# Performance work log

Hardware: AMD Instinct MI355X
Metric: run time of the kernel (lower is better)

## Reference

```python
import jax, jax.numpy as jnp
import numpy as np

B, S, D, DA, H = 4, 2048, 1024, 1024, 16
DH = DA // H  # 64, per-head dim (tensor_split on last dim == contiguous head chunks)


def setup_inputs() -> dict:
    key = jax.random.key(0)
    ks = jax.random.split(key, 8)
    init = 0.02
    return {
        "q": jax.random.normal(ks[0], (B, S, D), jnp.float32),
        "k": jax.random.normal(ks[1], (B, S, D), jnp.float32),
        "v": jax.random.normal(ks[2], (B, S, D), jnp.float32),
        "mask": jnp.ones((B, 1, S), jnp.int32),
        "w_q": jax.random.normal(ks[3], (DA, D), jnp.float32) * init,
        "b_q": jnp.zeros((DA,), jnp.float32),
        "w_k": jax.random.normal(ks[4], (DA, D), jnp.float32) * init,
        "b_k": jnp.zeros((DA,), jnp.float32),
        "w_v": jax.random.normal(ks[5], (DA, D), jnp.float32) * init,
        "b_v": jnp.zeros((DA,), jnp.float32),
        "w_o": jax.random.normal(ks[6], (D, DA), jnp.float32) * init,
        "b_o": jnp.zeros((D,), jnp.float32),
    }


def reference(q, k, v, mask, w_q, b_q, w_k, b_k, w_v, b_v, w_o, b_o):
    # projections (nn.Linear: x @ W.T + b)
    xq = q @ w_q.T + b_q            # [B,S,DA]
    xk = k @ w_k.T + b_k
    xv = v @ w_v.T + b_v
    # tensor_split into h contiguous chunks == reshape to [B,S,H,DH]
    xq = xq.reshape(B, S, H, DH)
    xk = xk.reshape(B, S, H, DH)
    xv = xv.reshape(B, S, H, DH)
    scores = jnp.einsum('bqhd,bkhd->bhqk', xq, xk) / jnp.sqrt(jnp.asarray(DH, xq.dtype))
    # mask [B,1,S] broadcasts over heads and query rows -> [B,1,1,S]
    scores = jnp.where(mask[:, None] == 0, -jnp.inf, scores)
    probs = jax.nn.softmax(scores, axis=-1)  # dropout p=0.0 -> identity
    out = jnp.einsum('bhqk,bkhd->bqhd', probs, xv).reshape(B, S, DA)
    return out @ w_o.T + b_o        # [B,S,D]
```

## Files before the change

### kernel.cpp

```cpp
#include <hip/hip_runtime.h>
#include <hip/hip_bf16.h>
#include <cstdint>
#include <cstddef>

typedef __bf16 bf16;
typedef __attribute__((ext_vector_type(8))) __bf16 bf16x8;
typedef __attribute__((ext_vector_type(4))) __bf16 bf16x4;
typedef __attribute__((ext_vector_type(4))) float f32x4;
typedef __attribute__((ext_vector_type(4))) int i32x4;

#define MFMA_BF16(a, b, c) __builtin_amdgcn_mfma_f32_16x16x32_bf16((a), (b), (c), 0, 0, 0)

constexpr int CB = 4;
constexpr int CS = 2048;
constexpr int CD = 1024;
constexpr int CDA = 1024;
constexpr int CH = 16;
constexpr int CM = CB * CS;
constexpr int NT = CS / 64;

__global__ __launch_bounds__(256) void cvt_w4(
    const float* __restrict__ s0, const float* __restrict__ s1,
    const float* __restrict__ s2, const float* __restrict__ s3,
    bf16* __restrict__ dst)
{
    int bid = blockIdx.x;
    int m = bid >> 9;
    size_t li = ((size_t)(bid & 511) * 256 + threadIdx.x) * 8;
    const float* s = (m == 0) ? s0 : (m == 1) ? s1 : (m == 2) ? s2 : s3;
    f32x4 a = *(const f32x4*)(s + li);
    f32x4 c = *(const f32x4*)(s + li + 4);
    bf16x8 o;
#pragma unroll
    for (int j = 0; j < 4; ++j) { o[j] = (bf16)a[j]; o[4 + j] = (bf16)c[j]; }
    *(bf16x8*)(dst + (size_t)m * (CD * CDA) + li) = o;
}

struct P3 {
    const float *A0, *A1, *A2;
    const float *b0, *b1, *b2;
    bf16 *C0, *C1, *C2;
};

__global__ __launch_bounds__(512, 2) void gemm_proj(P3 p, const bf16* __restrict__ Wb)
{
    __shared__ __align__(16) char smem[98304];

    const int t = threadIdx.x;
    const int lane = t & 63;
    const int wid = t >> 6;
    const int wr = wid >> 2, wc = wid & 3;
    const int l15 = lane & 15, lg = lane >> 4;
    const int m0 = blockIdx.x * 128;
    const int n0 = blockIdx.y * 256;
    const int z = blockIdx.z;

    const float* A    = (z == 0) ? p.A0 : (z == 1) ? p.A1 : p.A2;
    const float* bias = (z == 0) ? p.b0 : (z == 1) ? p.b1 : p.b2;
    const bf16*  W    = Wb + (size_t)z * (CD * CDA);

    const int arow = t >> 2, aq = t & 3;
    const float* asrc = A + (size_t)(m0 + arow) * CD + aq * 16;
    const int aoff0 = arow * 128 + (((2 * aq) ^ (arow & 7)) << 4);
    const int aoff1 = arow * 128 + (((2 * aq + 1) ^ (arow & 7)) << 4);
    const int brow_ = wid * 8 + (lane >> 3);
    const int bcol = ((lane & 7) ^ ((lane >> 3) & 7)) << 3;

    f32x4 av0, av1, av2, av3;

    auto ALOAD = [&](int k0) {
        av0 = *(const f32x4*)(asrc + k0);
        av1 = *(const f32x4*)(asrc + k0 + 4);
        av2 = *(const f32x4*)(asrc + k0 + 8);
        av3 = *(const f32x4*)(asrc + k0 + 12);
    };
    auto AWRITE = [&](int bufi) {
        char* Ab = smem + bufi * 16384;
        bf16x8 o0, o1;
#pragma unroll
        for (int jj = 0; jj < 4; ++jj) {
            o0[jj] = (bf16)av0[jj]; o0[4 + jj] = (bf16)av1[jj];
            o1[jj] = (bf16)av2[jj]; o1[4 + jj] = (bf16)av3[jj];
        }
        *(bf16x8*)(Ab + aoff0) = o0;
        *(bf16x8*)(Ab + aoff1) = o1;
    };
    auto BSTAGE = [&](int bufi, int k0) {
        char* Bb = smem + 32768 + bufi * 32768;
#pragma unroll
        for (int i = 0; i < 4; ++i) {
            const bf16* src = W + (size_t)(n0 + i * 64 + brow_) * CD + k0 + bcol;
            __builtin_amdgcn_global_load_lds(
                (const __attribute__((address_space(1))) void*)src,
                (__attribute__((address_space(3))) void*)(Bb + i * 8192 + wid * 1024),
                16, 0, 0);
        }
    };

    f32x4 acc[4][4] = {};

    ALOAD(0); BSTAGE(0, 0); AWRITE(0);
    __syncthreads();

    for (int ks = 0; ks < CD / 64; ++ks) {
        const int cur = ks & 1;
        if (ks + 1 < CD / 64) { BSTAGE(cur ^ 1, (ks + 1) * 64); ALOAD((ks + 1) * 64); }
        char* Ab = smem + cur * 16384;
        char* Bb = smem + 32768 + cur * 32768;
#pragma unroll
        for (int kk = 0; kk < 64; kk += 32) {
            bf16x8 af[4], bfv[4];
#pragma unroll
            for (int mi = 0; mi < 4; ++mi) {
                int row = wr * 64 + mi * 16 + l15;
                af[mi] = *(const bf16x8*)(Ab + row * 128 +
                                          ((((kk >> 3) + lg) ^ (row & 7)) << 4));
            }
#pragma unroll
            for (int ni = 0; ni < 4; ++ni) {
                int row = wc * 64 + ni * 16 + l15;
                bfv[ni] = *(const bf16x8*)(Bb + 128 * row +
                                           ((((kk >> 3) + lg) ^ (row & 7)) << 4));
            }
            __builtin_amdgcn_s_setprio(1);
#pragma unroll
            for (int mi = 0; mi < 4; ++mi)
#pragma unroll
                for (int ni = 0; ni < 4; ++ni)
                    acc[mi][ni] = MFMA_BF16(af[mi], bfv[ni], acc[mi][ni]);
            __builtin_amdgcn_s_setprio(0);
        }
        if (ks + 1 < CD / 64) AWRITE(cur ^ 1);
        __syncthreads();
    }

    if (z == 2) {
        bf16* C = p.C2;
        const int mblock = m0 + wr * 64;
#pragma unroll
        for (int ni = 0; ni < 4; ++ni) {
            int n = n0 + wc * 64 + ni * 16 + l15;
            float bv = bias[n];
#pragma unroll
            for (int mi = 0; mi < 4; ++mi) {
                int s = mi * 16 + lg * 4;
                int cps = (s & 32) | ((s & 12) << 1) | ((s & 16) >> 2);
                bf16x4 o;
#pragma unroll
                for (int r = 0; r < 4; ++r) o[r] = (bf16)(acc[mi][ni][r] + bv);
                *(bf16x4*)(C + (size_t)n * CM + mblock + cps) = o;
            }
        }
    } else {
        bf16* C = (z == 0) ? p.C0 : p.C1;
#pragma unroll
        for (int ni = 0; ni < 4; ++ni) {
            int col = n0 + wc * 64 + ni * 16 + l15;
            float bv = bias[col];
#pragma unroll
            for (int mi = 0; mi < 4; ++mi)
#pragma unroll
                for (int r = 0; r < 4; ++r) {
                    int row = m0 + wr * 64 + mi * 16 + lg * 4 + r;
                    C[(size_t)row * CDA + col] = (bf16)(acc[mi][ni][r] + bv);
                }
        }
    }
}

__global__ __launch_bounds__(512, 2) void gemm_out(
    const bf16* __restrict__ A, const bf16* __restrict__ W,
    const float* __restrict__ bias, float* __restrict__ C)
{
    __shared__ __align__(16) char smem[98304];

    const int t = threadIdx.x;
    const int lane = t & 63;
    const int wid = t >> 6;
    const int wr = wid >> 2, wc = wid & 3;
    const int l15 = lane & 15, lg = lane >> 4;
    const int m0 = blockIdx.x * 128;
    const int n0 = blockIdx.y * 256;

    const int grow_ = wid * 8 + (lane >> 3);
    const int gcol = ((lane & 7) ^ ((lane >> 3) & 7)) << 3;

    auto STAGE = [&](int bufi, int k0) {
        char* Ab = smem + bufi * 16384;
        char* Bb = smem + 32768 + bufi * 32768;
#pragma unroll
        for (int i = 0; i < 2; ++i) {
            const bf16* src = A + (size_t)(m0 + i * 64 + grow_) * CDA + k0 + gcol;
            __builtin_amdgcn_global_load_lds(
                (const __attribute__((address_space(1))) void*)src,
                (__attribute__((address_space(3))) void*)(Ab + i * 8192 + wid * 1024),
                16, 0, 0);
        }
#pragma unroll
        for (int i = 0; i < 4; ++i) {
            const bf16* src = W + (size_t)(n0 + i * 64 + grow_) * CDA + k0 + gcol;
            __builtin_amdgcn_global_load_lds(
                (const __attribute__((address_space(1))) void*)src,
                (__attribute__((address_space(3))) void*)(Bb + i * 8192 + wid * 1024),
                16, 0, 0);
        }
    };

    f32x4 acc[4][4] = {};

    STAGE(0, 0);
    __syncthreads();

    for (int ks = 0; ks < CDA / 64; ++ks) {
        const int cur = ks & 1;
        if (ks + 1 < CDA / 64) STAGE(cur ^ 1, (ks + 1) * 64);
        char* Ab = smem + cur * 16384;
        char* Bb = smem + 32768 + cur * 32768;
#pragma unroll
        for (int kk = 0; kk < 64; kk += 32) {
            bf16x8 af[4], bfv[4];
#pragma unroll
            for (int mi = 0; mi < 4; ++mi) {
                int row = wr * 64 + mi * 16 + l15;
                af[mi] = *(const bf16x8*)(Ab + row * 128 +
                                          ((((kk >> 3) + lg) ^ (row & 7)) << 4));
            }
#pragma unroll
            for (int ni = 0; ni < 4; ++ni) {
                int row = wc * 64 + ni * 16 + l15;
                bfv[ni] = *(const bf16x8*)(Bb + 128 * row +
                                           ((((kk >> 3) + lg) ^ (row & 7)) << 4));
            }
            __builtin_amdgcn_s_setprio(1);
#pragma unroll
            for (int mi = 0; mi < 4; ++mi)
#pragma unroll
                for (int ni = 0; ni < 4; ++ni)
                    acc[mi][ni] = MFMA_BF16(af[mi], bfv[ni], acc[mi][ni]);
            __builtin_amdgcn_s_setprio(0);
        }
        __syncthreads();
    }

#pragma unroll
    for (int ni = 0; ni < 4; ++ni) {
        int col = n0 + wc * 64 + ni * 16 + l15;
        float bv = bias[col];
#pragma unroll
        for (int mi = 0; mi < 4; ++mi)
#pragma unroll
            for (int r = 0; r < 4; ++r) {
                int row = m0 + wr * 64 + mi * 16 + lg * 4 + r;
                C[(size_t)row * CD + col] = acc[mi][ni][r] + bv;
            }
    }
}

__global__ __launch_bounds__(512, 4) void attn_kernel(
    const bf16* __restrict__ xq, const bf16* __restrict__ xk,
    const bf16* __restrict__ xvT, const int* __restrict__ mask,
    bf16* __restrict__ out)
{
    __shared__ __align__(16) char smem[40960];
    float* Mb = (float*)(smem + 32768);

    const int t = threadIdx.x;
    const int lane = t & 63;
    const int wid = t >> 6;
    const int l15 = lane & 15, lg = lane >> 4;
    const int g = blockIdx.x;
    const int j = g >> 3;
    const int bh = (g & 7) * 8 + (j & 7);
    const int qt = j >> 3;
    const int b = bh >> 4, h = bh & 15;
    const int q0 = qt * 256;
    constexpr float SCL = 0.125f * 1.44269504088896340736f;
    constexpr float M2 = 12.0f * SCL;

    const int sub = lane >> 3;
    const int sb  = (lane & 7) ^ sub;
    const bf16* kbase = xk + (size_t)(b * CS + wid * 8 + sub) * CDA + h * 64 + sb * 8;
    const bf16* vbase = xvT + (size_t)(h * 64 + wid * 8 + sub) * CM + b * CS + sb * 8;

#define STAGE(bufi, ktt)                                                           \
    {                                                                              \
        char* Kd = smem + (bufi) * 16384 + wid * 1024;                             \
        char* Vd = smem + (bufi) * 16384 + 8192 + wid * 1024;                      \
        __builtin_amdgcn_global_load_lds(                                          \
            (const __attribute__((address_space(1))) void*)(kbase + (size_t)(ktt) * 64 * CDA), \
            (__attribute__((address_space(3))) void*)Kd, 16, 0, 0);                \
        __builtin_amdgcn_global_load_lds(                                          \
            (const __attribute__((address_space(1))) void*)(vbase + (ktt) * 64),   \
            (__attribute__((address_space(3))) void*)Vd, 16, 0, 0);                \
    }

    {
        i32x4 mk = *(const i32x4*)(mask + b * CS + t * 4);
        f32x4 o;
#pragma unroll
        for (int r = 0; r < 4; ++r) o[r] = (mk[r] == 0) ? -1.0e30f : -M2;
        *(f32x4*)(Mb + t * 4) = o;
    }

    bf16x8 aq[2][2];
#pragma unroll
    for (int mi = 0; mi < 2; ++mi)
#pragma unroll
        for (int kh = 0; kh < 2; ++kh) {
            bf16x8 v = *(const bf16x8*)(xq +
                (size_t)(b * CS + q0 + wid * 32 + mi * 16 + l15) * CDA + h * 64 + kh * 32 + lg * 8);
#pragma unroll
            for (int jj = 0; jj < 8; ++jj) v[jj] = (bf16)((float)v[jj] * SCL);
            aq[mi][kh] = v;
        }

    bf16x8 onescol;
    {
        bf16 fv = (l15 == 0) ? (bf16)1.0f : (bf16)0.0f;
#pragma unroll
        for (int jj = 0; jj < 8; ++jj) onescol[jj] = fv;
    }

    int koff[2][4], voff[2][4];
#pragma unroll
    for (int kh = 0; kh < 2; ++kh)
#pragma unroll
        for (int ni = 0; ni < 4; ++ni) {
            int key = ni * 16 + l15;
            koff[kh][ni] = key * 128 + ((kh * 64 + lg * 16) ^ ((key & 7) << 4));
        }
#pragma unroll
    for (int kks = 0; kks < 2; ++kks)
#pragma unroll
        for (int di = 0; di < 4; ++di) {
            int d = di * 16 + l15;
            voff[kks][di] = 8192 + d * 128 + ((kks * 64 + lg * 16) ^ ((d & 7) << 4));
        }

    f32x4 accO[2][5] = {};

    STAGE(0, 0);
    __syncthreads();

    for (int kt = 0; kt < NT; ++kt) {
        const int cur = kt & 1;
        char* buf = smem + cur * 16384;

        if (kt + 1 < NT) STAGE(cur ^ 1, kt + 1);

        f32x4 mb[4];
#pragma unroll
        for (int ni = 0; ni < 4; ++ni)
            mb[ni] = *(const f32x4*)(Mb + kt * 64 + ni * 16 + lg * 4);

        f32x4 sT[4][2];
#pragma unroll
        for (int ni = 0; ni < 4; ++ni) { sT[ni][0] = mb[ni]; sT[ni][1] = mb[ni]; }
#pragma unroll
        for (int kh = 0; kh < 2; ++kh) {
            bf16x8 bk[4];
#pragma unroll
            for (int ni = 0; ni < 4; ++ni)
                bk[ni] = *(const bf16x8*)(buf + koff[kh][ni]);
            __builtin_amdgcn_s_setprio(1);
#pragma unroll
            for (int ni = 0; ni < 4; ++ni)
#pragma unroll
                for (int mi = 0; mi < 2; ++mi)
                    sT[ni][mi] = MFMA_BF16(bk[ni], aq[mi][kh], sT[ni][mi]);
            __builtin_amdgcn_s_setprio(0);
        }

#pragma unroll
        for (int ni = 0; ni < 4; ++ni)
#pragma unroll
            for (int mi = 0; mi < 2; ++mi)
#pragma unroll
                for (int r = 0; r < 4; ++r)
                    sT[ni][mi][r] = exp2f(sT[ni][mi][r]);

        bf16x8 ap[2][2];
#pragma unroll
        for (int kks = 0; kks < 2; ++kks)
#pragma unroll
            for (int mi = 0; mi < 2; ++mi)
#pragma unroll
                for (int r = 0; r < 4; ++r) {
                    ap[kks][mi][r]     = (bf16)sT[2 * kks][mi][r];
                    ap[kks][mi][4 + r] = (bf16)sT[2 * kks + 1][mi][r];
                }

#pragma unroll
        for (int kks = 0; kks < 2; ++kks) {
            bf16x8 bv[4];
#pragma unroll
            for (int di = 0; di < 4; ++di)
                bv[di] = *(const bf16x8*)(buf + voff[kks][di]);
            __builtin_amdgcn_s_setprio(1);
#pragma unroll
            for (int mi = 0; mi < 2; ++mi) {
#pragma unroll
                for (int di = 0; di < 4; ++di)
                    accO[mi][di] = MFMA_BF16(ap[kks][mi], bv[di], accO[mi][di]);
                accO[mi][4] = MFMA_BF16(ap[kks][mi], onescol, accO[mi][4]);
            }
            __builtin_amdgcn_s_setprio(0);
        }

        __syncthreads();
    }
#undef STAGE

    char* Ob = smem + wid * 2048;
#pragma unroll
    for (int mi = 0; mi < 2; ++mi) {
#pragma unroll
        for (int r = 0; r < 4; ++r) {
            float lsum = __shfl(accO[mi][4][r], lane & 48);
            float inv = 1.0f / lsum;
            int qr = lg * 4 + r;
#pragma unroll
            for (int di = 0; di < 4; ++di)
                *(bf16*)(Ob + qr * 128 + (((di * 16 + l15) * 2) ^ ((qr & 7) << 4))) =
                    (bf16)(accO[mi][di][r] * inv);
        }
        __builtin_amdgcn_sched_barrier(0);
#pragma unroll
        for (int i = 0; i < 2; ++i) {
            int rr = i * 8 + (lane >> 3);
            int ch = lane & 7;
            bf16x8 o = *(const bf16x8*)(Ob + rr * 128 + ((ch * 16) ^ ((rr & 7) << 4)));
            *(bf16x8*)(out + (size_t)(b * CS + q0 + wid * 32 + mi * 16 + rr) * CDA +
                       h * 64 + ch * 8) = o;
        }
        __builtin_amdgcn_sched_barrier(0);
    }
}

extern "C" void kernel_launch(void* const* d_in, const int* in_sizes, int n_in,
                              void* d_out, int out_size, void* d_ws, size_t ws_size,
                              hipStream_t stream)
{
    const float* q   = (const float*)d_in[0];
    const float* k   = (const float*)d_in[1];
    const float* v   = (const float*)d_in[2];
    const int*   msk = (const int*)d_in[3];
    const float* w_q = (const float*)d_in[4];
    const float* b_q = (const float*)d_in[5];
    const float* w_k = (const float*)d_in[6];
    const float* b_k = (const float*)d_in[7];
    const float* w_v = (const float*)d_in[8];
    const float* b_v = (const float*)d_in[9];
    const float* w_o = (const float*)d_in[10];
    const float* b_o = (const float*)d_in[11];

    bf16* xq  = (bf16*)d_ws;
    bf16* xk  = xq + (size_t)CM * CDA;
    bf16* xvT = xk + (size_t)CM * CDA;
    bf16* at  = xvT + (size_t)CM * CDA;
    bf16* wb  = at + (size_t)CM * CDA;

    cvt_w4<<<dim3(2048), 256, 0, stream>>>(w_q, w_k, w_v, w_o, wb);

    P3 p{q, k, v, b_q, b_k, b_v, xq, xk, xvT};
    gemm_proj<<<dim3(CM / 128, CDA / 256, 3), 512, 0, stream>>>(p, wb);

    attn_kernel<<<dim3(512), 512, 0, stream>>>(xq, xk, xvT, msk, at);

    gemm_out<<<dim3(CM / 128, CD / 256), 512, 0, stream>>>(
        at, wb + 3 * (size_t)(CD * CDA), b_o, (float*)d_out);
}
```

Baseline: 195.0 us.

## Replace double-buffered projection GEMM with single-buffer K=128 tiles

The QKV projection GEMM drops its two-stage double-buffered pipeline (K=64 per stage, prefetching the next A/B tiles) in favour of one shared-memory buffer holding K=128 tiles, with load, sync, compute and sync in each iteration. This halves the number of loop iterations and barriers and simplifies register use, but global loads no longer overlap MFMA work within a block, so latency hiding depends on the other resident block per CU. The swizzle and row stride are adjusted to the 256-byte rows.

```diff
diff --git a/kernel.cpp b/kernel.cpp
--- a/kernel.cpp
+++ b/kernel.cpp
@@ -60,66 +60,55 @@
     const bf16*  W    = Wb + (size_t)z * (CD * CDA);
 
     const int arow = t >> 2, aq = t & 3;
-    const float* asrc = A + (size_t)(m0 + arow) * CD + aq * 16;
-    const int aoff0 = arow * 128 + (((2 * aq) ^ (arow & 7)) << 4);
-    const int aoff1 = arow * 128 + (((2 * aq + 1) ^ (arow & 7)) << 4);
-    const int brow_ = wid * 8 + (lane >> 3);
-    const int bcol = ((lane & 7) ^ ((lane >> 3) & 7)) << 3;
-
-    f32x4 av0, av1, av2, av3;
-
-    auto ALOAD = [&](int k0) {
-        av0 = *(const f32x4*)(asrc + k0);
-        av1 = *(const f32x4*)(asrc + k0 + 4);
-        av2 = *(const f32x4*)(asrc + k0 + 8);
-        av3 = *(const f32x4*)(asrc + k0 + 12);
-    };
-    auto AWRITE = [&](int bufi) {
-        char* Ab = smem + bufi * 16384;
-        bf16x8 o0, o1;
-#pragma unroll
-        for (int jj = 0; jj < 4; ++jj) {
-            o0[jj] = (bf16)av0[jj]; o0[4 + jj] = (bf16)av1[jj];
-            o1[jj] = (bf16)av2[jj]; o1[4 + jj] = (bf16)av3[jj];
-        }
-        *(bf16x8*)(Ab + aoff0) = o0;
-        *(bf16x8*)(Ab + aoff1) = o1;
-    };
-    auto BSTAGE = [&](int bufi, int k0) {
-        char* Bb = smem + 32768 + bufi * 32768;
-#pragma unroll
-        for (int i = 0; i < 4; ++i) {
-            const bf16* src = W + (size_t)(n0 + i * 64 + brow_) * CD + k0 + bcol;
+    const float* asrc = A + (size_t)(m0 + arow) * CD + aq * 32;
+    int aoff[4];
+#pragma unroll
+    for (int j = 0; j < 4; ++j)
+        aoff[j] = arow * 256 + (((aq * 4 + j) ^ (arow & 7)) << 4);
+
+    const int bhi = lane >> 4;
+    const size_t bsrcoff = (size_t)bhi * CD +
+                           (((lane & 15) ^ ((wid & 1) * 4 + bhi)) << 3);
+
+    char* Ab = smem;
+    char* Bb = smem + 32768;
+
+    f32x4 acc[4][4] = {};
+
+    for (int ks = 0; ks < CD / 128; ++ks) {
+        const int k0 = ks * 128;
+#pragma unroll
+        for (int j = 0; j < 4; ++j) {
+            f32x4 v0 = *(const f32x4*)(asrc + k0 + j * 8);
+            f32x4 v1 = *(const f32x4*)(asrc + k0 + j * 8 + 4);
+            bf16x8 o;
+#pragma unroll
+            for (int jj = 0; jj < 4; ++jj) { o[jj] = (bf16)v0[jj]; o[4 + jj] = (bf16)v1[jj]; }
+            *(bf16x8*)(Ab + aoff[j]) = o;
+        }
+#pragma unroll
+        for (int i = 0; i < 8; ++i) {
+            const bf16* src = W + (size_t)(n0 + i * 32 + wid * 4) * CD + k0 + bsrcoff;
             __builtin_amdgcn_global_load_lds(
                 (const __attribute__((address_space(1))) void*)src,
                 (__attribute__((address_space(3))) void*)(Bb + i * 8192 + wid * 1024),
                 16, 0, 0);
         }
-    };
-
-    f32x4 acc[4][4] = {};
-
-    ALOAD(0); BSTAGE(0, 0); AWRITE(0);
-    __syncthreads();
-
-    for (int ks = 0; ks < CD / 64; ++ks) {
-        const int cur = ks & 1;
-        if (ks + 1 < CD / 64) { BSTAGE(cur ^ 1, (ks + 1) * 64); ALOAD((ks + 1) * 64); }
-        char* Ab = smem + cur * 16384;
-        char* Bb = smem + 32768 + cur * 32768;
-#pragma unroll
-        for (int kk = 0; kk < 64; kk += 32) {
+        __syncthreads();
+
+#pragma unroll
+        for (int kk = 0; kk < 128; kk += 32) {
             bf16x8 af[4], bfv[4];
 #pragma unroll
             for (int mi = 0; mi < 4; ++mi) {
                 int row = wr * 64 + mi * 16 + l15;
-                af[mi] = *(const bf16x8*)(Ab + row * 128 +
+                af[mi] = *(const bf16x8*)(Ab + row * 256 +
                                           ((((kk >> 3) + lg) ^ (row & 7)) << 4));
             }
 #pragma unroll
             for (int ni = 0; ni < 4; ++ni) {
                 int row = wc * 64 + ni * 16 + l15;
-                bfv[ni] = *(const bf16x8*)(Bb + 128 * row +
+                bfv[ni] = *(const bf16x8*)(Bb + row * 256 +
                                            ((((kk >> 3) + lg) ^ (row & 7)) << 4));
             }
             __builtin_amdgcn_s_setprio(1);
@@ -130,7 +119,6 @@
                     acc[mi][ni] = MFMA_BF16(af[mi], bfv[ni], acc[mi][ni]);
             __builtin_amdgcn_s_setprio(0);
         }
-        if (ks + 1 < CD / 64) AWRITE(cur ^ 1);
         __syncthreads();
     }
 
```

Result: slower. 225.4 us (+15.6%).
